# Performance work log

Hardware: AMD Instinct MI355X
Metric: run time of the kernel (lower is better)

## Reference

```python
import jax, jax.numpy as jnp
import numpy as np
from jax import lax

DIM = 512
HEADS = 8
DIM_HEAD = 64          # dim // 8
LANDMARKS = 256        # dim // 2
PINV_ITERS = 6
KERNEL = 33            # residual depthwise conv kernel (lucidrains default)
LN_EPS = 1e-5


def setup_inputs() -> dict:
    key = jax.random.key(0)
    ks = jax.random.split(key, 5)
    b, n = 4, 8192
    x = jax.random.normal(ks[0], (b, n, DIM), jnp.float32)
    ln_w = jnp.ones((DIM,), jnp.float32)
    ln_b = jnp.zeros((DIM,), jnp.float32)
    w_qkv = jax.random.normal(ks[1], (DIM, 3 * HEADS * DIM_HEAD), jnp.float32) * (DIM ** -0.5)
    w_out = jax.random.normal(ks[2], (HEADS * DIM_HEAD, DIM), jnp.float32) * (DIM ** -0.5)
    b_out = jnp.zeros((DIM,), jnp.float32)
    conv_w = jax.random.normal(ks[3], (HEADS, 1, KERNEL, 1), jnp.float32) * 0.05
    return {"x": x, "ln_w": ln_w, "ln_b": ln_b, "w_qkv": w_qkv,
            "w_out": w_out, "b_out": b_out, "conv_w": conv_w}


def _moore_penrose_pinv(a, iters):
    # iterative Moore-Penrose pseudoinverse (Ben-Israel/Cohen cubic scheme)
    abs_a = jnp.abs(a)
    # global max over all batch/head slices, matching torch.max(col)*torch.max(row)
    scale = jnp.max(abs_a.sum(-1)) * jnp.max(abs_a.sum(-2))
    z = jnp.swapaxes(a, -1, -2) / scale
    I = jnp.eye(a.shape[-1], dtype=a.dtype)
    for _ in range(iters):
        az = a @ z
        z = 0.25 * (z @ (13.0 * I - az @ (11.0 * I - az @ (7.0 * I - az))))
    return z


def reference(x, ln_w, ln_b, w_qkv, w_out, b_out, conv_w):
    b, n, d = x.shape
    h, dh, m = HEADS, DIM_HEAD, LANDMARKS
    # --- LayerNorm ---
    mu = jnp.mean(x, -1, keepdims=True)
    var = jnp.mean((x - mu) ** 2, -1, keepdims=True)
    xn = (x - mu) * lax.rsqrt(var + LN_EPS) * ln_w + ln_b
    # --- pad front so seq divisible by num_landmarks (static; 0 here) ---
    pad = (-n) % m
    xp = jnp.pad(xn, ((0, 0), (pad, 0), (0, 0)))
    npad = n + pad
    # --- qkv projections ---
    qkv = xp @ w_qkv                      # (b, npad, 3*h*dh)
    q, k, v = jnp.split(qkv, 3, axis=-1)
    to_heads = lambda t: t.reshape(b, npad, h, dh).transpose(0, 2, 1, 3)  # bhnd
    q = to_heads(q) * (dh ** -0.5)
    k = to_heads(k)
    v = to_heads(v)
    # --- landmarks: mean over contiguous blocks of length l ---
    l = npad // m
    q_l = q.reshape(b, h, m, l, dh).mean(3)   # (b,h,m,dh)
    k_l = k.reshape(b, h, m, l, dh).mean(3)
    # --- three similarity/softmax blocks ---
    a1 = jax.nn.softmax(jnp.einsum('bhid,bhjd->bhij', q, k_l), -1)   # (b,h,n,m)
    a2 = jax.nn.softmax(jnp.einsum('bhid,bhjd->bhij', q_l, k_l), -1) # (b,h,m,m)
    a3 = jax.nn.softmax(jnp.einsum('bhid,bhjd->bhij', q_l, k), -1)   # (b,h,m,n)
    out = (a1 @ _moore_penrose_pinv(a2, PINV_ITERS)) @ (a3 @ v)      # (b,h,n,dh)
    # --- depthwise conv residual on v along sequence axis ---
    res = lax.conv_general_dilated(
        v, conv_w, window_strides=(1, 1),
        padding=((KERNEL // 2, KERNEL // 2), (0, 0)),
        dimension_numbers=('NCHW', 'OIHW', 'NCHW'),
        feature_group_count=h)
    out = out + res
    # --- merge heads, output projection, strip pad (dropout = identity in eval) ---
    out = out.transpose(0, 2, 1, 3).reshape(b, npad, h * dh)
    out = out @ w_out + b_out
    out = out[:, npad - n:]
    # --- TransLayer residual ---
    return x + out
```

## Files before the change

kernel.cpp:

```cpp
#include <hip/hip_runtime.h>

#define DEV __device__ __forceinline__

typedef unsigned short u16;
typedef unsigned int   u32;
typedef u16   u16x8 __attribute__((ext_vector_type(8)));
typedef __bf16 bf16x8 __attribute__((ext_vector_type(8)));
typedef float f32x4 __attribute__((ext_vector_type(4)));

DEV float b2f(u16 u){ return __uint_as_float(((u32)u) << 16); }
DEV u16 f2b(float f){ u32 u = __float_as_uint(f); u32 r = (u + 0x7fffu + ((u >> 16) & 1u)) >> 16; return (u16)r; }

DEV f32x4 mfma16(u16x8 a, u16x8 b, f32x4 c){
  return __builtin_amdgcn_mfma_f32_16x16x32_bf16(
      __builtin_bit_cast(bf16x8, a), __builtin_bit_cast(bf16x8, b), c, 0, 0, 0);
}

DEV void gload16(const void* g, void* l){
  __builtin_amdgcn_global_load_lds(
      (const __attribute__((address_space(1))) u32*)g,
      (__attribute__((address_space(3))) u32*)l,
      16, 0, 0);
}

__global__ __launch_bounds__(256) void ln_kernel(const float* __restrict__ x,
                                                 const float* __restrict__ w,
                                                 const float* __restrict__ bb,
                                                 u16* __restrict__ xn,
                                                 float2* __restrict__ stats){
  int row = blockIdx.x;
  const float* xr = x + (size_t)row * 512;
  int t = threadIdx.x;
  float2 v = *(const float2*)(xr + t * 2);
  float s = v.x + v.y;
  float sq = v.x * v.x + v.y * v.y;
  #pragma unroll
  for(int off = 32; off; off >>= 1){ s += __shfl_xor(s, off, 64); sq += __shfl_xor(sq, off, 64); }
  __shared__ float rs[4], rq[4];
  int wv = t >> 6, ln = t & 63;
  if(ln == 0){ rs[wv] = s; rq[wv] = sq; }
  __syncthreads();
  s = rs[0] + rs[1] + rs[2] + rs[3];
  sq = rq[0] + rq[1] + rq[2] + rq[3];
  float mu = s * (1.f / 512.f);
  float var = sq * (1.f / 512.f) - mu * mu;
  float rstd = rsqrtf(var + 1e-5f);
  if(t == 0) stats[row] = make_float2(mu, rstd);
  float w0 = w[t * 2], w1 = w[t * 2 + 1], b0 = bb[t * 2], b1 = bb[t * 2 + 1];
  u16 u0 = f2b((v.x - mu) * rstd * w0 + b0);
  u16 u1 = f2b((v.y - mu) * rstd * w1 + b1);
  ((u32*)(xn + (size_t)row * 512))[t] = (u32)u0 | ((u32)u1 << 16);
}

__global__ __launch_bounds__(256) void xl_kernel(const float* __restrict__ x,
                                                 const float2* __restrict__ stats,
                                                 const float* __restrict__ w,
                                                 const float* __restrict__ bb,
                                                 float* __restrict__ xl){
  int blk = blockIdx.x;
  int b = blk >> 8, j = blk & 255;
  int t = threadIdx.x;
  int d0 = t * 2;
  float acc0 = 0.f, acc1 = 0.f;
  size_t row0 = (size_t)b * 8192 + (size_t)j * 32;
  for(int tt = 0; tt < 32; tt++){
    size_t row = row0 + tt;
    float2 st = stats[row];
    const float* xr = x + row * 512;
    float2 v = *(const float2*)(xr + d0);
    acc0 += (v.x - st.x) * st.y;
    acc1 += (v.y - st.x) * st.y;
  }
  float* dst = xl + (size_t)blk * 512;
  dst[d0]     = acc0 * (1.f / 32.f) * w[d0]     + bb[d0];
  dst[d0 + 1] = acc1 * (1.f / 32.f) * w[d0 + 1] + bb[d0 + 1];
}

__global__ __launch_bounds__(256) void trans_kernel(const float* __restrict__ src,
                                                    u16* __restrict__ dst, int K, int N){
  int idx = blockIdx.x * 256 + threadIdx.x;
  if(idx >= K * N) return;
  int k = idx / N, n = idx - k * N;
  dst[(size_t)n * K + k] = f2b(src[idx]);
}

__global__ __launch_bounds__(256) void transf32_kernel(const float* __restrict__ src,
                                                       float* __restrict__ dst){
  int idx = blockIdx.x * 256 + threadIdx.x;
  int n = idx >> 9, k = idx & 511;
  dst[idx] = src[(size_t)k * 1536 + n];
}

__global__ __launch_bounds__(256) void vtrans_kernel(const u16* __restrict__ v,
                                                     u16* __restrict__ vt){
  __shared__ u16 tile[64][72];
  int bh = blockIdx.y, n0 = blockIdx.x * 64;
  int t = threadIdx.x;
  for(int s = t; s < 512; s += 256){
    int row = s >> 3, col = (s & 7) * 8;
    *(u16x8*)&tile[row][col] = *(const u16x8*)(v + ((size_t)bh * 8192 + n0 + row) * 64 + col);
  }
  __syncthreads();
  for(int s = t; s < 512; s += 256){
    int d = s >> 3, nc = (s & 7) * 8;
    u16x8 u;
    #pragma unroll
    for(int e = 0; e < 8; e++) u[e] = tile[nc + e][d];
    *(u16x8*)(vt + ((size_t)bh * 64 + d) * 8192 + n0 + nc) = u;
  }
}

template<int EPI>
__global__ __launch_bounds__(256) void gemm128(const u16* __restrict__ A,
                                               const u16* __restrict__ BT,
                                               u16* __restrict__ qo, u16* __restrict__ ko, u16* __restrict__ vo,
                                               const float* __restrict__ bout,
                                               const float* __restrict__ xres,
                                               float* __restrict__ dout){
  __shared__ u16 As[128 * 32];
  __shared__ u16 Bs[128 * 32];
  const int K = 512;
  int tb_m = blockIdx.x * 128, tb_n = blockIdx.y * 128;
  int tid = threadIdx.x, lane = tid & 63, w = tid >> 6;
  int wm = (w >> 1) * 64, wn = (w & 1) * 64;
  f32x4 acc[4][4] = {};
  int srow = tid >> 2, sk = (tid & 3) * 8;
  const u16* Ag = A + (size_t)(tb_m + srow) * K + sk;
  const u16* Bg = BT + (size_t)(tb_n + srow) * K + sk;
  u16* Al = As + tid * 8;
  u16* Bl = Bs + tid * 8;
  for(int kk = 0; kk < K; kk += 32){
    __syncthreads();
    gload16(Ag + kk, Al);
    gload16(Ag + kk + (size_t)64 * K, Al + 2048);
    gload16(Bg + kk, Bl);
    gload16(Bg + kk + (size_t)64 * K, Bl + 2048);
    __syncthreads();
    int r = lane & 15, ko2 = (lane >> 4) * 8;
    u16x8 af[4], bf[4];
    #pragma unroll
    for(int mi = 0; mi < 4; mi++) af[mi] = *(const u16x8*)&As[(wm + mi * 16 + r) * 32 + ko2];
    #pragma unroll
    for(int ni = 0; ni < 4; ni++) bf[ni] = *(const u16x8*)&Bs[(wn + ni * 16 + r) * 32 + ko2];
    #pragma unroll
    for(int mi = 0; mi < 4; mi++)
      #pragma unroll
      for(int ni = 0; ni < 4; ni++)
        acc[mi][ni] = mfma16(af[mi], bf[ni], acc[mi][ni]);
  }
  int r = lane & 15, rr = (lane >> 4) * 4;
  #pragma unroll
  for(int mi = 0; mi < 4; mi++)
    #pragma unroll
    for(int ni = 0; ni < 4; ni++){
      int col = tb_n + wn + ni * 16 + r;
      #pragma unroll
      for(int e = 0; e < 4; e++){
        int row = tb_m + wm + mi * 16 + rr + e;
        float val = acc[mi][ni][e];
        if(EPI == 0){
          int t3 = col >> 9, h = (col >> 6) & 7, dh = col & 63;
          int b = row >> 13, n = row & 8191;
          if(t3 == 0) val *= 0.125f;
          u16* dst = (t3 == 0 ? qo : (t3 == 1 ? ko : vo));
          dst[(((size_t)(b * 8 + h) * 8192) + n) * 64 + dh] = f2b(val);
        } else {
          val += bout[col] + xres[(size_t)row * 512 + col];
          dout[(size_t)row * 512 + col] = val;
        }
      }
    }
}

__global__ __launch_bounds__(256) void gemm_qlkl(const float* __restrict__ A,
                                                 const float* __restrict__ BT,
                                                 float* __restrict__ qlf,
                                                 float* __restrict__ klf,
                                                 u16* __restrict__ qlh, u16* __restrict__ qll,
                                                 u16* __restrict__ klh, u16* __restrict__ kll){
  __shared__ float As[64][17];
  __shared__ float Bs[64][17];
  int tb_m = blockIdx.x * 64, tb_n = blockIdx.y * 64;
  int tid = threadIdx.x;
  int ty = tid >> 4, tx = tid & 15;
  float acc[4][4] = {};
  int srow = tid >> 2, sseg = (tid & 3) * 4;
  const float* Ag = A + (size_t)(tb_m + srow) * 512 + sseg;
  const float* Bg = BT + (size_t)(tb_n + srow) * 512 + sseg;
  for(int kk = 0; kk < 512; kk += 16){
    __syncthreads();
    f32x4 a4 = *(const f32x4*)(Ag + kk);
    f32x4 b4 = *(const f32x4*)(Bg + kk);
    #pragma unroll
    for(int e = 0; e < 4; e++){ As[srow][sseg + e] = a4[e]; Bs[srow][sseg + e] = b4[e]; }
    __syncthreads();
    #pragma unroll
    for(int k2 = 0; k2 < 16; k2++){
      float a[4], b[4];
      #pragma unroll
      for(int i = 0; i < 4; i++) a[i] = As[ty * 4 + i][k2];
      #pragma unroll
      for(int jv = 0; jv < 4; jv++) b[jv] = Bs[tx * 4 + jv][k2];
      #pragma unroll
      for(int i = 0; i < 4; i++)
        #pragma unroll
        for(int jv = 0; jv < 4; jv++) acc[i][jv] += a[i] * b[jv];
    }
  }
  #pragma unroll
  for(int i = 0; i < 4; i++)
    #pragma unroll
    for(int jv = 0; jv < 4; jv++){
      int r = tb_m + ty * 4 + i;
      int c = tb_n + tx * 4 + jv;
      int b = r >> 8, jl = r & 255;
      float val = acc[i][jv];
      if(c < 512){
        float q = val * 0.125f;
        size_t qi = (((size_t)(b * 8 + (c >> 6)) * 256) + jl) * 64 + (c & 63);
        qlf[qi] = q;
        u16 hi = f2b(q);
        qlh[qi] = hi; qll[qi] = f2b(q - b2f(hi));
      } else {
        int c2 = c - 512;
        size_t ki = (((size_t)(b * 8 + (c2 >> 6)) * 256) + jl) * 64 + (c2 & 63);
        klf[ki] = val;
        u16 hi = f2b(val);
        klh[ki] = hi; kll[ki] = f2b(val - b2f(hi));
      }
    }
}

__global__ __launch_bounds__(256) void gemm_pinv_f32(const float* __restrict__ A,
                                                     const float* __restrict__ B,
                                                     float* __restrict__ C,
                                                     float dB, float sB, float osc){
  __shared__ float As[64][68];
  __shared__ float Bs[64][68];
  int bh = blockIdx.y;
  size_t base = (size_t)bh * 65536;
  int tb_m = (blockIdx.x >> 2) * 64, tb_n = (blockIdx.x & 3) * 64;
  int tid = threadIdx.x;
  int ty = tid >> 4, tx = tid & 15;
  float acc[4][4] = {};
  int arow = tid >> 2, acol = (tid & 3) * 16;
  int brow = tid >> 3, bcol = (tid & 7) * 8;
  const float* Ag = A + base + (size_t)(tb_m + arow) * 256 + acol;
  const float* Bg = B + base + (size_t)brow * 256 + tb_n + bcol;
  for(int kk = 0; kk < 256; kk += 64){
    f32x4 a[4];
    #pragma unroll
    for(int q = 0; q < 4; q++) a[q] = *(const f32x4*)(Ag + kk + q * 4);
    f32x4 b[2][2];
    #pragma unroll
    for(int rr = 0; rr < 2; rr++){
      const float* bp = Bg + (size_t)(kk + rr * 32) * 256;
      b[rr][0] = *(const f32x4*)bp;
      b[rr][1] = *(const f32x4*)(bp + 4);
    }
    __syncthreads();
    #pragma unroll
    for(int q = 0; q < 4; q++)
      #pragma unroll
      for(int e = 0; e < 4; e++)
        As[acol + q * 4 + e][arow] = a[q][e];
    #pragma unroll
    for(int rr = 0; rr < 2; rr++){
      int krow = kk + rr * 32 + brow;
      f32x4 v0, v1;
      #pragma unroll
      for(int e = 0; e < 4; e++){
        float t0 = sB * b[rr][0][e]; if(krow == tb_n + bcol + e)     t0 += dB;
        float t1 = sB * b[rr][1][e]; if(krow == tb_n + bcol + 4 + e) t1 += dB;
        v0[e] = t0; v1[e] = t1;
      }
      *(f32x4*)&Bs[rr * 32 + brow][bcol]     = v0;
      *(f32x4*)&Bs[rr * 32 + brow][bcol + 4] = v1;
    }
    __syncthreads();
    #pragma unroll
    for(int k2 = 0; k2 < 64; k2++){
      f32x4 av4 = *(const f32x4*)&As[k2][ty * 4];
      f32x4 bv4 = *(const f32x4*)&Bs[k2][tx * 4];
      #pragma unroll
      for(int i = 0; i < 4; i++)
        #pragma unroll
        for(int jv = 0; jv < 4; jv++) acc[i][jv] += av4[i] * bv4[jv];
    }
  }
  #pragma unroll
  for(int i = 0; i < 4; i++){
    int r = tb_m + ty * 4 + i;
    f32x4 ov;
    #pragma unroll
    for(int jv = 0; jv < 4; jv++) ov[jv] = osc * acc[i][jv];
    *(f32x4*)(C + base + (size_t)r * 256 + tb_n + tx * 4) = ov;
  }
}

__global__ __launch_bounds__(256) void a2_kernel(const float* __restrict__ qlf,
                                                 const float* __restrict__ klf,
                                                 float* __restrict__ a2){
  int i = blockIdx.x, bh = blockIdx.y, j = threadIdx.x;
  const float* qp = qlf + ((size_t)bh * 256 + i) * 64;
  const float* kp = klf + ((size_t)bh * 256 + j) * 64;
  float s = 0.f;
  #pragma unroll
  for(int d0 = 0; d0 < 16; d0++){
    f32x4 uq = *(const f32x4*)(qp + d0 * 4);
    f32x4 uk = *(const f32x4*)(kp + d0 * 4);
    #pragma unroll
    for(int e = 0; e < 4; e++) s += uq[e] * uk[e];
  }
  __shared__ float red[256];
  red[j] = s; __syncthreads();
  for(int off = 128; off; off >>= 1){ if(j < off) red[j] = fmaxf(red[j], red[j + off]); __syncthreads(); }
  float m = red[0]; __syncthreads();
  float p = expf(s - m);
  red[j] = p; __syncthreads();
  for(int off = 128; off; off >>= 1){ if(j < off) red[j] += red[j + off]; __syncthreads(); }
  float denom = red[0];
  a2[((size_t)bh * 256 + i) * 256 + j] = p / denom;
}

__global__ __launch_bounds__(256) void scale_kernel(const float* __restrict__ a2, u32* __restrict__ maxes){
  int bh = blockIdx.x, t = threadIdx.x;
  const float* p = a2 + (size_t)bh * 65536;
  float cs = 0.f, rs = 0.f;
  for(int i = 0; i < 256; i++) cs += p[i * 256 + t];
  for(int j = 0; j < 256; j++) rs += p[t * 256 + j];
  __shared__ float rc[256], rr[256];
  rc[t] = cs; rr[t] = rs; __syncthreads();
  for(int off = 128; off; off >>= 1){
    if(t < off){ rc[t] = fmaxf(rc[t], rc[t + off]); rr[t] = fmaxf(rr[t], rr[t + off]); }
    __syncthreads();
  }
  if(t == 0){
    atomicMax(&maxes[0], __float_as_uint(rc[0]));
    atomicMax(&maxes[1], __float_as_uint(rr[0]));
  }
}

__global__ __launch_bounds__(256) void z0_kernel(const float* __restrict__ a2,
                                                 float* __restrict__ z,
                                                 const u32* __restrict__ maxes){
  __shared__ float tile[64][65];
  float inv = 1.f / (__uint_as_float(maxes[0]) * __uint_as_float(maxes[1]));
  int bh = blockIdx.z;
  int i0 = blockIdx.x * 64, j0 = blockIdx.y * 64;
  const float* src = a2 + (size_t)bh * 65536;
  float* dst = z + (size_t)bh * 65536;
  for(int s = threadIdx.x; s < 1024; s += 256){
    int r = s >> 4, c4 = (s & 15) * 4;
    f32x4 v = *(const f32x4*)(src + (size_t)(i0 + r) * 256 + j0 + c4);
    #pragma unroll
    for(int e = 0; e < 4; e++) tile[r][c4 + e] = v[e];
  }
  __syncthreads();
  for(int s = threadIdx.x; s < 1024; s += 256){
    int jr = s >> 4, c4 = (s & 15) * 4;
    f32x4 v;
    #pragma unroll
    for(int e = 0; e < 4; e++) v[e] = tile[c4 + e][jr] * inv;
    *(f32x4*)(dst + (size_t)(j0 + jr) * 256 + i0 + c4) = v;
  }
}

template<int MODE>
__global__ __launch_bounds__(256) void flash_kernel(
    const u16* __restrict__ Aex,
    const u16* __restrict__ Ah_, const u16* __restrict__ Al_,
    const u16* __restrict__ Bh_, const u16* __restrict__ Bl_,
    const u16* __restrict__ Vh_, const u16* __restrict__ Vl_,
    u16* __restrict__ o,
    float* __restrict__ pacc, float* __restrict__ plo){
  extern __shared__ char smem[];
  u32 (*pbuf)[32][35] = (u32(*)[32][35])smem;
  u16 (*ksh)[72] = (u16(*)[72])(smem + 17920);
  u16 (*vsh)[72] = (u16(*)[72])(smem + 17920 + 9216);
  u16 (*ksl)[72] = (u16(*)[72])(smem + 17920 + 2 * 9216);
  u16 (*vsl)[72] = (u16(*)[72])(smem + 17920 + 3 * 9216);

  int tid = threadIdx.x;
  int w = tid >> 6, lane = tid & 63;
  int lr = lane & 15, lg = lane >> 4;
  int bh = blockIdx.y;
  int rowbase = blockIdx.x * 128 + w * 32;
  constexpr int NT = (MODE == 0) ? 4 : 8;
  int kbase = (MODE == 0) ? 0 : blockIdx.z * 512;
  int srow = tid >> 2, sseg = (tid & 3) * 16;

  u16x8 afh[2][2], afl[2][2];
  #pragma unroll
  for(int mi = 0; mi < 2; mi++)
    #pragma unroll
    for(int ks = 0; ks < 2; ks++){
      int r = rowbase + mi * 16 + lr;
      if(MODE == 0){
        afh[mi][ks] = *(const u16x8*)(Aex + ((size_t)bh * 8192 + r) * 64 + ks * 32 + lg * 8);
      } else {
        size_t idx = ((size_t)bh * 256 + r) * 64 + ks * 32 + lg * 8;
        afh[mi][ks] = *(const u16x8*)(Ah_ + idx);
        afl[mi][ks] = *(const u16x8*)(Al_ + idx);
      }
    }

  f32x4 pv[2][4] = {};
  float l[2][4] = {};

  for(int t = 0; t < NT; t++){
    int koff = t * 64;
    __syncthreads();
    if(MODE == 0){
      size_t kix = ((size_t)bh * 256 + koff + srow) * 64 + sseg;
      *(u16x8*)&ksh[srow][sseg]     = *(const u16x8*)(Bh_ + kix);
      *(u16x8*)&ksh[srow][sseg + 8] = *(const u16x8*)(Bh_ + kix + 8);
      *(u16x8*)&ksl[srow][sseg]     = *(const u16x8*)(Bl_ + kix);
      *(u16x8*)&ksl[srow][sseg + 8] = *(const u16x8*)(Bl_ + kix + 8);
      size_t vix = ((size_t)bh * 64 + srow) * 256 + koff + sseg;
      *(u16x8*)&vsh[srow][sseg]     = *(const u16x8*)(Vh_ + vix);
      *(u16x8*)&vsh[srow][sseg + 8] = *(const u16x8*)(Vh_ + vix + 8);
      *(u16x8*)&vsl[srow][sseg]     = *(const u16x8*)(Vl_ + vix);
      *(u16x8*)&vsl[srow][sseg + 8] = *(const u16x8*)(Vl_ + vix + 8);
    } else {
      size_t kix = ((size_t)bh * 8192 + kbase + koff + srow) * 64 + sseg;
      *(u16x8*)&ksh[srow][sseg]     = *(const u16x8*)(Bh_ + kix);
      *(u16x8*)&ksh[srow][sseg + 8] = *(const u16x8*)(Bh_ + kix + 8);
      size_t vix = ((size_t)bh * 64 + srow) * 8192 + kbase + koff + sseg;
      *(u16x8*)&vsh[srow][sseg]     = *(const u16x8*)(Vh_ + vix);
      *(u16x8*)&vsh[srow][sseg + 8] = *(const u16x8*)(Vh_ + vix + 8);
    }
    __syncthreads();
    #pragma unroll
    for(int half = 0; half < 2; half++){
      u16x8 bfh[2][2], bfl[2][2];
      #pragma unroll
      for(int ni = 0; ni < 2; ni++){
        int krow = half * 32 + ni * 16 + lr;
        #pragma unroll
        for(int ks = 0; ks < 2; ks++){
          bfh[ni][ks] = *(const u16x8*)&ksh[krow][ks * 32 + lg * 8];
          if(MODE == 0) bfl[ni][ks] = *(const u16x8*)&ksl[krow][ks * 32 + lg * 8];
        }
      }
      f32x4 sv[2][2];
      #pragma unroll
      for(int mi = 0; mi < 2; mi++)
        #pragma unroll
        for(int ni = 0; ni < 2; ni++) sv[mi][ni] = (f32x4){0.f, 0.f, 0.f, 0.f};
      #pragma unroll
      for(int ks = 0; ks < 2; ks++)
        #pragma unroll
        for(int mi = 0; mi < 2; mi++)
          #pragma unroll
          for(int ni = 0; ni < 2; ni++){
            sv[mi][ni] = mfma16(afh[mi][ks], bfh[ni][ks], sv[mi][ni]);
            if(MODE == 0) sv[mi][ni] = mfma16(afh[mi][ks], bfl[ni][ks], sv[mi][ni]);
            else          sv[mi][ni] = mfma16(afl[mi][ks], bfh[ni][ks], sv[mi][ni]);
          }
      #pragma unroll
      for(int mi = 0; mi < 2; mi++)
        #pragma unroll
        for(int ni = 0; ni < 2; ni++)
          #pragma unroll
          for(int e = 0; e < 4; e++){
            float p = __expf(sv[mi][ni][e]);
            l[mi][e] += p;
            u32 pb = __float_as_uint(p);
            u32 rb = pb + 0x7fffu + ((pb >> 16) & 1u);
            float hif = __uint_as_float(rb & 0xffff0000u);
            u32 lob = __float_as_uint(p - hif);
            pbuf[w][mi * 16 + lg * 4 + e][ni * 16 + lr] = __builtin_amdgcn_perm(lob, rb, 0x07060302u);
          }
      u16x8 pah[2], pal[2];
      #pragma unroll
      for(int mi = 0; mi < 2; mi++){
        u32 tv[8];
        #pragma unroll
        for(int e2 = 0; e2 < 8; e2++) tv[e2] = pbuf[w][mi * 16 + lr][lg * 8 + e2];
        u32* ph = (u32*)&pah[mi];
        u32* pl = (u32*)&pal[mi];
        #pragma unroll
        for(int q = 0; q < 4; q++){
          ph[q] = __builtin_amdgcn_perm(tv[2 * q + 1], tv[2 * q], 0x05040100u);
          pl[q] = __builtin_amdgcn_perm(tv[2 * q + 1], tv[2 * q], 0x07060302u);
        }
      }
      #pragma unroll
      for(int ni2 = 0; ni2 < 4; ni2++){
        int d = ni2 * 16 + lr;
        u16x8 vh = *(const u16x8*)&vsh[d][half * 32 + lg * 8];
        u16x8 vl;
        if(MODE == 0) vl = *(const u16x8*)&vsl[d][half * 32 + lg * 8];
        #pragma unroll
        for(int mi = 0; mi < 2; mi++){
          pv[mi][ni2] = mfma16(pah[mi], vh, pv[mi][ni2]);
          if(MODE == 0){
            pv[mi][ni2] = mfma16(pah[mi], vl, pv[mi][ni2]);
            pv[mi][ni2] = mfma16(pal[mi], vh, pv[mi][ni2]);
          } else {
            pv[mi][ni2] = mfma16(pal[mi], vh, pv[mi][ni2]);
          }
        }
      }
    }
  }
  #pragma unroll
  for(int mi = 0; mi < 2; mi++)
    #pragma unroll
    for(int e = 0; e < 4; e++){
      float lv = l[mi][e];
      #pragma unroll
      for(int off = 1; off < 16; off <<= 1) lv += __shfl_xor(lv, off, 64);
      l[mi][e] = lv;
    }
  #pragma unroll
  for(int mi = 0; mi < 2; mi++){
    #pragma unroll
    for(int e = 0; e < 4; e++){
      int row = rowbase + mi * 16 + lg * 4 + e;
      if(MODE == 0){
        float invl = 1.f / l[mi][e];
        int b = bh >> 3, h = bh & 7;
        #pragma unroll
        for(int ni2 = 0; ni2 < 4; ni2++){
          int col = ni2 * 16 + lr;
          size_t oi = ((size_t)b * 8192 + row) * 512 + h * 64 + col;
          o[oi] = f2b(pv[mi][ni2][e] * invl + b2f(o[oi]));
        }
      } else {
        #pragma unroll
        for(int ni2 = 0; ni2 < 4; ni2++){
          int col = ni2 * 16 + lr;
          pacc[(((size_t)blockIdx.z * 8192) + (size_t)bh * 256 + row) * 64 + col] = pv[mi][ni2][e];
        }
      }
    }
  }
  if(MODE == 1 && lr == 0){
    #pragma unroll
    for(int mi = 0; mi < 2; mi++)
      #pragma unroll
      for(int e = 0; e < 4; e++){
        int row = rowbase + mi * 16 + lg * 4 + e;
        plo[(size_t)blockIdx.z * 8192 + (size_t)bh * 256 + row] = l[mi][e];
      }
  }
}

__global__ __launch_bounds__(64) void a3v_merge(const float* __restrict__ pacc,
                                                const float* __restrict__ plo,
                                                float* __restrict__ av){
  int row = blockIdx.x, d = threadIdx.x;
  float L = 0.f, acc = 0.f;
  #pragma unroll
  for(int p = 0; p < 16; p++){
    L += plo[(size_t)p * 8192 + row];
    acc += pacc[((size_t)p * 8192 + row) * 64 + d];
  }
  av[(size_t)row * 64 + d] = acc / L;
}

__global__ __launch_bounds__(64) void zw_kernel(const float* __restrict__ z,
                                                const float* __restrict__ av,
                                                u16* __restrict__ wth, u16* __restrict__ wtl){
  int i = blockIdx.x & 255, bh = blockIdx.x >> 8, d = threadIdx.x;
  const float* zr = z + ((size_t)bh * 256 + i) * 256;
  const float* ab = av + (size_t)bh * 256 * 64;
  float s = 0.f;
  for(int j = 0; j < 256; j++) s += zr[j] * ab[j * 64 + d];
  size_t oi = ((size_t)bh * 64 + d) * 256 + i;
  u16 hi = f2b(s);
  wth[oi] = hi;
  wtl[oi] = f2b(s - b2f(hi));
}

__global__ __launch_bounds__(256) void conv_kernel(const u16* __restrict__ v,
                                                   const float* __restrict__ cw,
                                                   u16* __restrict__ o){
  __shared__ float wl[33];
  __shared__ float vt[64][104];
  int bh = blockIdx.y, b = bh >> 3, h = bh & 7;
  int r0 = blockIdx.x * 64;
  if(threadIdx.x < 33) wl[threadIdx.x] = cw[h * 33 + threadIdx.x];
  const u16* vb = v + (size_t)bh * 8192 * 64;
  for(int idx = threadIdx.x; idx < 768; idx += 256){
    int row = idx >> 3, c8 = (idx & 7) * 8;
    int gr = r0 - 16 + row;
    u16x8 u = {};
    if(gr >= 0 && gr < 8192) u = *(const u16x8*)(vb + (size_t)gr * 64 + c8);
    #pragma unroll
    for(int e = 0; e < 8; e++) vt[c8 + e][row] = b2f(u[e]);
  }
  __syncthreads();
  int d = threadIdx.x & 63, g = threadIdx.x >> 6;
  float vin[48];
  #pragma unroll
  for(int i = 0; i < 12; i++){
    f32x4 q4 = *(const f32x4*)&vt[d][g * 16 + i * 4];
    #pragma unroll
    for(int e = 0; e < 4; e++) vin[i * 4 + e] = q4[e];
  }
  float acc[16] = {};
  #pragma unroll
  for(int t = 0; t < 33; t++){
    float wt = wl[t];
    #pragma unroll
    for(int r = 0; r < 16; r++) acc[r] += wt * vin[r + t];
  }
  #pragma unroll
  for(int r = 0; r < 16; r++){
    size_t oi = ((size_t)b * 8192 + (r0 + g * 16 + r)) * 512 + h * 64 + d;
    o[oi] = f2b(acc[r]);
  }
}

extern "C" void kernel_launch(void* const* d_in, const int* in_sizes, int n_in,
                              void* d_out, int out_size, void* d_ws, size_t ws_size,
                              hipStream_t stream){
  (void)in_sizes; (void)n_in; (void)out_size; (void)ws_size;
  const float* x     = (const float*)d_in[0];
  const float* ln_w  = (const float*)d_in[1];
  const float* ln_b  = (const float*)d_in[2];
  const float* w_qkv = (const float*)d_in[3];
  const float* w_out = (const float*)d_in[4];
  const float* b_out = (const float*)d_in[5];
  const float* cw    = (const float*)d_in[6];
  float* out = (float*)d_out;

  char* base = (char*)d_ws;
  size_t off = 0;
  auto alloc = [&](size_t bytes)->void*{
    void* r = base + off; off += (bytes + 255) & ~(size_t)255; return r;
  };
  u16* xn      = (u16*)alloc(32768ull * 512 * 2);
  float2* stat = (float2*)alloc(32768ull * 8);
  u16* qb      = (u16*)alloc(32ull * 8192 * 64 * 2);
  u16* kb      = (u16*)alloc(32ull * 8192 * 64 * 2);
  u16* vb      = (u16*)alloc(32ull * 8192 * 64 * 2);
  u16* vtb     = (u16*)alloc(32ull * 8192 * 64 * 2);
  u16* wqkvT   = (u16*)alloc(1536ull * 512 * 2);
  u16* woutT   = (u16*)alloc(512ull * 512 * 2);
  float* wqkT  = (float*)alloc(1024ull * 512 * 4);
  float* xl    = (float*)alloc(1024ull * 512 * 4);
  float* qlf   = (float*)alloc(32ull * 256 * 64 * 4);
  float* klf   = (float*)alloc(32ull * 256 * 64 * 4);
  u16* qlh     = (u16*)alloc(32ull * 256 * 64 * 2);
  u16* qll     = (u16*)alloc(32ull * 256 * 64 * 2);
  u16* klh     = (u16*)alloc(32ull * 256 * 64 * 2);
  u16* kll     = (u16*)alloc(32ull * 256 * 64 * 2);
  float* a2b   = (float*)alloc(32ull * 65536 * 4);
  float* zA    = (float*)alloc(32ull * 65536 * 4);
  float* zB    = (float*)alloc(32ull * 65536 * 4);
  float* az    = (float*)alloc(32ull * 65536 * 4);
  float* x2    = (float*)alloc(32ull * 65536 * 4);
  float* x3    = (float*)alloc(32ull * 65536 * 4);
  float* av    = (float*)alloc(32ull * 256 * 64 * 4);
  u16* wth     = (u16*)alloc(32ull * 64 * 256 * 2);
  u16* wtl     = (u16*)alloc(32ull * 64 * 256 * 2);
  u32* scal    = (u32*)alloc(256);
  u16* ob = xn;
  float* pacc = zB;
  float* plo  = a2b;

  hipMemsetAsync(scal, 0, 8, stream);
  ln_kernel<<<32768, 256, 0, stream>>>(x, ln_w, ln_b, xn, stat);
  trans_kernel<<<3072, 256, 0, stream>>>(w_qkv, wqkvT, 512, 1536);
  trans_kernel<<<1024, 256, 0, stream>>>(w_out, woutT, 512, 512);
  transf32_kernel<<<2048, 256, 0, stream>>>(w_qkv, wqkT);
  gemm128<0><<<dim3(256, 12), 256, 0, stream>>>(xn, wqkvT, qb, kb, vb, nullptr, nullptr, nullptr);
  vtrans_kernel<<<dim3(128, 32), 256, 0, stream>>>(vb, vtb);
  xl_kernel<<<1024, 256, 0, stream>>>(x, stat, ln_w, ln_b, xl);
  gemm_qlkl<<<dim3(16, 16), 256, 0, stream>>>(xl, wqkT, qlf, klf, qlh, qll, klh, kll);
  a2_kernel<<<dim3(256, 32), 256, 0, stream>>>(qlf, klf, a2b);
  scale_kernel<<<32, 256, 0, stream>>>(a2b, scal);
  z0_kernel<<<dim3(4, 4, 32), 256, 0, stream>>>(a2b, zA, scal);

  float* zP = zA; float* zQ = zB;
  for(int it = 0; it < 6; it++){
    gemm_pinv_f32<<<dim3(16, 32), 256, 0, stream>>>(a2b, zP, az, 0.f, 1.f, 1.f);
    gemm_pinv_f32<<<dim3(16, 32), 256, 0, stream>>>(az, az, x2, 7.f, -1.f, 1.f);
    gemm_pinv_f32<<<dim3(16, 32), 256, 0, stream>>>(az, x2, x3, 11.f, -1.f, 1.f);
    gemm_pinv_f32<<<dim3(16, 32), 256, 0, stream>>>(zP, x3, zQ, 13.f, -1.f, 0.25f);
    float* t1 = zP; zP = zQ; zQ = t1;
  }

  flash_kernel<1><<<dim3(2, 32, 16), 256, 36352, stream>>>(nullptr, qlh, qll, kb, nullptr, vtb, nullptr,
                                                           nullptr, pacc, plo);
  a3v_merge<<<8192, 64, 0, stream>>>(pacc, plo, av);
  zw_kernel<<<8192, 64, 0, stream>>>(zP, av, wth, wtl);
  conv_kernel<<<dim3(128, 32), 256, 0, stream>>>(vb, cw, ob);
  flash_kernel<0><<<dim3(64, 32), 256, 54784, stream>>>(qb, nullptr, nullptr, klh, kll, wth, wtl,
                                                        ob, nullptr, nullptr);
  gemm128<1><<<dim3(256, 4), 256, 0, stream>>>(ob, woutT, nullptr, nullptr, nullptr, b_out, x, out);
}
```

Before: 961.3 us.

## Prefetch next K/V tile into registers while computing current tile

The attention tile loop now loads the next K/V tile from global memory into registers while the current tile is computed from shared memory. It then stores that tile to LDS after a barrier, giving a two-stage software pipeline. The intent is to hide global load latency behind the MFMA work. The cost is more live registers, which may lower occupancy, and the manual unroll by two assumes an even tile count. A small unroll pragma is also added to the zw reduction loop.

```diff
diff --git a/kernel.cpp b/kernel.cpp
--- a/kernel.cpp
+++ b/kernel.cpp
@@ -408,29 +408,41 @@
   f32x4 pv[2][4] = {};
   float l[2][4] = {};
 
-  for(int t = 0; t < NT; t++){
+  auto LOADT = [&](int t, u16x8* rk, u16x8* rkl, u16x8* rv, u16x8* rvl){
     int koff = t * 64;
-    __syncthreads();
     if(MODE == 0){
       size_t kix = ((size_t)bh * 256 + koff + srow) * 64 + sseg;
-      *(u16x8*)&ksh[srow][sseg]     = *(const u16x8*)(Bh_ + kix);
-      *(u16x8*)&ksh[srow][sseg + 8] = *(const u16x8*)(Bh_ + kix + 8);
-      *(u16x8*)&ksl[srow][sseg]     = *(const u16x8*)(Bl_ + kix);
-      *(u16x8*)&ksl[srow][sseg + 8] = *(const u16x8*)(Bl_ + kix + 8);
+      rk[0]  = *(const u16x8*)(Bh_ + kix);
+      rk[1]  = *(const u16x8*)(Bh_ + kix + 8);
+      rkl[0] = *(const u16x8*)(Bl_ + kix);
+      rkl[1] = *(const u16x8*)(Bl_ + kix + 8);
       size_t vix = ((size_t)bh * 64 + srow) * 256 + koff + sseg;
-      *(u16x8*)&vsh[srow][sseg]     = *(const u16x8*)(Vh_ + vix);
-      *(u16x8*)&vsh[srow][sseg + 8] = *(const u16x8*)(Vh_ + vix + 8);
-      *(u16x8*)&vsl[srow][sseg]     = *(const u16x8*)(Vl_ + vix);
-      *(u16x8*)&vsl[srow][sseg + 8] = *(const u16x8*)(Vl_ + vix + 8);
+      rv[0]  = *(const u16x8*)(Vh_ + vix);
+      rv[1]  = *(const u16x8*)(Vh_ + vix + 8);
+      rvl[0] = *(const u16x8*)(Vl_ + vix);
+      rvl[1] = *(const u16x8*)(Vl_ + vix + 8);
     } else {
       size_t kix = ((size_t)bh * 8192 + kbase + koff + srow) * 64 + sseg;
-      *(u16x8*)&ksh[srow][sseg]     = *(const u16x8*)(Bh_ + kix);
-      *(u16x8*)&ksh[srow][sseg + 8] = *(const u16x8*)(Bh_ + kix + 8);
+      rk[0] = *(const u16x8*)(Bh_ + kix);
+      rk[1] = *(const u16x8*)(Bh_ + kix + 8);
       size_t vix = ((size_t)bh * 64 + srow) * 8192 + kbase + koff + sseg;
-      *(u16x8*)&vsh[srow][sseg]     = *(const u16x8*)(Vh_ + vix);
-      *(u16x8*)&vsh[srow][sseg + 8] = *(const u16x8*)(Vh_ + vix + 8);
-    }
-    __syncthreads();
+      rv[0] = *(const u16x8*)(Vh_ + vix);
+      rv[1] = *(const u16x8*)(Vh_ + vix + 8);
+    }
+  };
+  auto STORET = [&](const u16x8* rk, const u16x8* rkl, const u16x8* rv, const u16x8* rvl){
+    *(u16x8*)&ksh[srow][sseg]     = rk[0];
+    *(u16x8*)&ksh[srow][sseg + 8] = rk[1];
+    *(u16x8*)&vsh[srow][sseg]     = rv[0];
+    *(u16x8*)&vsh[srow][sseg + 8] = rv[1];
+    if(MODE == 0){
+      *(u16x8*)&ksl[srow][sseg]     = rkl[0];
+      *(u16x8*)&ksl[srow][sseg + 8] = rkl[1];
+      *(u16x8*)&vsl[srow][sseg]     = rvl[0];
+      *(u16x8*)&vsl[srow][sseg + 8] = rvl[1];
+    }
+  };
+  auto COMPUTE = [&](){
     #pragma unroll
     for(int half = 0; half < 2; half++){
       u16x8 bfh[2][2], bfl[2][2];
@@ -504,7 +516,24 @@
         }
       }
     }
-  }
+  };
+
+  u16x8 rkA[2], rklA[2], rvA[2], rvlA[2];
+  u16x8 rkB[2], rklB[2], rvB[2], rvlB[2];
+  LOADT(0, rkA, rklA, rvA, rvlA);
+  for(int tt = 0; tt < NT; tt += 2){
+    __syncthreads();
+    STORET(rkA, rklA, rvA, rvlA);
+    if(tt + 1 < NT) LOADT(tt + 1, rkB, rklB, rvB, rvlB);
+    __syncthreads();
+    COMPUTE();
+    __syncthreads();
+    STORET(rkB, rklB, rvB, rvlB);
+    if(tt + 2 < NT) LOADT(tt + 2, rkA, rklA, rvA, rvlA);
+    __syncthreads();
+    COMPUTE();
+  }
+
   #pragma unroll
   for(int mi = 0; mi < 2; mi++)
     #pragma unroll
@@ -568,6 +597,7 @@
   const float* zr = z + ((size_t)bh * 256 + i) * 256;
   const float* ab = av + (size_t)bh * 256 * 64;
   float s = 0.f;
+  #pragma unroll 4
   for(int j = 0; j < 256; j++) s += zr[j] * ab[j * 64 + d];
   size_t oi = ((size_t)bh * 64 + d) * 256 + i;
   u16 hi = f2b(s);
```

After: 1.010 ms. 1.05x slower.
